# Kernel optimization log

Hardware: AMD Instinct MI355X
Metric: run time of the kernel (lower is better)

## Reference

```python
import jax, jax.numpy as jnp
import numpy as np

T = 8192
N_EMBD = 1024
HEAD_SIZE = 64
NEG_FILL = -1e9


def setup_inputs() -> dict:
    key = jax.random.key(0)
    kq, kk, kv, kwq, kwk, kwv = jax.random.split(key, 6)
    s = 1.0 / np.sqrt(N_EMBD)
    return {
        "encodings_for_q": jax.random.normal(kq, (T, N_EMBD), dtype=jnp.float32),
        "encodings_for_k": jax.random.normal(kk, (T, N_EMBD), dtype=jnp.float32),
        "encodings_for_v": jax.random.normal(kv, (T, N_EMBD), dtype=jnp.float32),
        # causal mask: True above the diagonal -> positions to mask out
        "mask": jnp.triu(jnp.ones((T, T), dtype=bool), k=1),
        # torch Linear weights have shape [out_features, in_features]
        "W_q": jax.random.normal(kwq, (HEAD_SIZE, N_EMBD), dtype=jnp.float32) * s,
        "W_k": jax.random.normal(kwk, (HEAD_SIZE, N_EMBD), dtype=jnp.float32) * s,
        "W_v": jax.random.normal(kwv, (HEAD_SIZE, N_EMBD), dtype=jnp.float32) * s,
    }


def reference(encodings_for_q, encodings_for_k, encodings_for_v, mask, W_q, W_k, W_v):
    # projections: x @ W.T  (torch nn.Linear, bias=False)
    q = jnp.einsum("te,he->th", encodings_for_q, W_q)  # [T, H]
    k = jnp.einsum("te,he->th", encodings_for_k, W_k)  # [T, H]
    v = jnp.einsum("te,he->th", encodings_for_v, W_v)  # [T, H]
    scale = 1.0 / jnp.sqrt(jnp.asarray(HEAD_SIZE, dtype=q.dtype))
    sims = jnp.einsum("th,sh->ts", q, k) * scale       # [T, T]
    sims = jnp.where(mask, jnp.asarray(NEG_FILL, dtype=sims.dtype), sims)
    attn = jax.nn.softmax(sims, axis=1)                # softmax over col_dim=1
    return jnp.einsum("ts,sh->th", attn, v)            # [T, H]
```

## Files before the change

### kernel.cpp

```cpp
#include <hip/hip_runtime.h>
#include <hip/hip_bf16.h>
#include <stdint.h>

#define T_DIM 8192
#define E_DIM 1024
#define H_DIM 64
#define NEGF  -3.0e38f

typedef __attribute__((ext_vector_type(8))) short bf16x8;
typedef __attribute__((ext_vector_type(4))) float f32x4;

static __device__ __forceinline__ uint32_t pk2(float x, float y) {
    __hip_bfloat162 h = __float22bfloat162_rn(make_float2(x, y));
    union { __hip_bfloat162 h2; uint32_t u; } c; c.h2 = h; return c.u;
}
static __device__ __forceinline__ bf16x8 pack8(float4 a, float4 b) {
    union { bf16x8 v; uint32_t u[4]; } c;
    c.u[0] = pk2(a.x, a.y); c.u[1] = pk2(a.z, a.w);
    c.u[2] = pk2(b.x, b.y); c.u[3] = pk2(b.z, b.w);
    return c.v;
}
static __device__ __forceinline__ uint16_t bf1(float x) {
    __hip_bfloat16 h = __float2bfloat16(x);
    union { __hip_bfloat16 h1; uint16_t s; } c; c.h1 = h; return c.s;
}

__global__ __launch_bounds__(256) void wconv_kernel(
    const float* __restrict__ Wq, const float* __restrict__ Wk, const float* __restrict__ Wv,
    uint16_t* __restrict__ Wqb, uint16_t* __restrict__ Wkb, uint16_t* __restrict__ Wvb)
{
    const int idx = blockIdx.x * 256 + threadIdx.x;
    const int which = idx / 16384;
    const int off = (idx & 16383) * 4;
    const float* W = (which == 0) ? Wq : (which == 1) ? Wk : Wv;
    uint16_t* Wb   = (which == 0) ? Wqb : (which == 1) ? Wkb : Wvb;
    float4 w = *(const float4*)(W + off);
    uint2 o = make_uint2(pk2(w.x, w.y), pk2(w.z, w.w));
    *(uint2*)(Wb + off) = o;
}

__global__ __launch_bounds__(256) void proj_kernel(
    const float* __restrict__ Xq, const float* __restrict__ Xk, const float* __restrict__ Xv,
    const uint16_t* __restrict__ Wqb, const uint16_t* __restrict__ Wkb, const uint16_t* __restrict__ Wvb,
    uint16_t* __restrict__ Qb, uint16_t* __restrict__ Kb, uint16_t* __restrict__ Vtb)
{
    __shared__ float TD[64][69];

    const int mat = blockIdx.y;
    const float* X    = (mat == 0) ? Xq  : (mat == 1) ? Xk  : Xv;
    const uint16_t* W = (mat == 0) ? Wqb : (mat == 1) ? Wkb : Wvb;

    const int tid  = threadIdx.x;
    const int wv   = tid >> 6;
    const int lane = tid & 63;
    const int lidx = lane & 15;
    const int quad = lane >> 4;
    const int t0   = blockIdx.x * 64 + wv * 16;

    const float* Xr = X + (size_t)(t0 + lidx) * E_DIM + quad * 8;

    f32x4 acc[4] = {{0,0,0,0},{0,0,0,0},{0,0,0,0},{0,0,0,0}};
    for (int k0 = 0; k0 < E_DIM; k0 += 32) {
        float4 x0 = *(const float4*)(Xr + k0);
        float4 x1 = *(const float4*)(Xr + k0 + 4);
        bf16x8 xa = pack8(x0, x1);
        #pragma unroll
        for (int nt = 0; nt < 4; ++nt) {
            const uint16_t* Wr = W + (size_t)(nt * 16 + lidx) * E_DIM + k0 + quad * 8;
            bf16x8 wb = *(const bf16x8*)Wr;
            acc[nt] = __builtin_amdgcn_mfma_f32_16x16x32_bf16(xa, wb, acc[nt], 0, 0, 0);
        }
    }

    if (mat < 2) {
        uint16_t* O = (mat == 0) ? Qb : Kb;
        #pragma unroll
        for (int nt = 0; nt < 4; ++nt)
            #pragma unroll
            for (int r = 0; r < 4; ++r)
                O[(size_t)(t0 + quad * 4 + r) * H_DIM + nt * 16 + lidx] = bf1(acc[nt][r]);
    } else {
        #pragma unroll
        for (int nt = 0; nt < 4; ++nt)
            #pragma unroll
            for (int r = 0; r < 4; ++r)
                TD[wv * 16 + quad * 4 + r][nt * 16 + lidx] = acc[nt][r];
        __syncthreads();
        const int h = tid >> 2, tq = tid & 3;
        uint32_t w8[8];
        #pragma unroll
        for (int i = 0; i < 8; ++i)
            w8[i] = pk2(TD[tq * 16 + 2 * i][h], TD[tq * 16 + 2 * i + 1][h]);
        uint16_t* dst = Vtb + (size_t)h * T_DIM + blockIdx.x * 64 + tq * 16;
        uint4 lo = make_uint4(w8[0], w8[1], w8[2], w8[3]);
        uint4 hi = make_uint4(w8[4], w8[5], w8[6], w8[7]);
        *(uint4*)dst       = lo;
        *(uint4*)(dst + 8) = hi;
    }
}

__global__ __launch_bounds__(512) void flash_kernel(
    const uint16_t* __restrict__ Qb, const uint16_t* __restrict__ Kb,
    const uint16_t* __restrict__ Vtb, float* __restrict__ Out)
{
    __shared__ __align__(16) float WS[8][16][68];
    __shared__ float Mw[8][16];
    __shared__ float Lw[8][16];

    const int tid  = threadIdx.x;
    const int wv   = tid >> 6;
    const int lane = tid & 63;
    const int lidx = lane & 15;
    const int quad = lane >> 4;

    const int qt = 511 - (int)blockIdx.x;
    const int q0 = qt * 16;

    bf16x8 aq0 = *(const bf16x8*)(Qb + (size_t)(q0 + lidx) * H_DIM + quad * 8);
    bf16x8 aq1 = *(const bf16x8*)(Qb + (size_t)(q0 + lidx) * H_DIM + 32 + quad * 8);

    const int ktiles  = qt / 4 + 1;
    const int base    = ktiles >> 3;
    const int rem     = ktiles & 7;
    const int myn     = base + (wv < rem ? 1 : 0);
    const int mystart = wv * base + (wv < rem ? wv : rem);

    float m[4] = {NEGF, NEGF, NEGF, NEGF};
    float l[4] = {0.f, 0.f, 0.f, 0.f};
    f32x4 o[4] = {{0,0,0,0},{0,0,0,0},{0,0,0,0},{0,0,0,0}};

    for (int it = 0; it < myn; ++it) {
        const int kt = mystart + it;
        const int s0 = kt * 64;

        f32x4 s[4];
        #pragma unroll
        for (int nt = 0; nt < 4; ++nt) {
            const uint16_t* kr = Kb + (size_t)(s0 + nt * 16 + lidx) * H_DIM + quad * 8;
            bf16x8 b0 = *(const bf16x8*)(kr);
            bf16x8 b1 = *(const bf16x8*)(kr + 32);
            f32x4 z = {0, 0, 0, 0};
            s[nt] = __builtin_amdgcn_mfma_f32_16x16x32_bf16(aq0, b0, z, 0, 0, 0);
            s[nt] = __builtin_amdgcn_mfma_f32_16x16x32_bf16(aq1, b1, s[nt], 0, 0, 0);
        }

        if (kt == ktiles - 1) {
            #pragma unroll
            for (int nt = 0; nt < 4; ++nt)
                #pragma unroll
                for (int r = 0; r < 4; ++r) {
                    const int col = s0 + nt * 16 + lidx;
                    const int row = q0 + quad * 4 + r;
                    s[nt][r] = (col <= row) ? s[nt][r] * 0.125f : NEGF;
                }
        } else {
            #pragma unroll
            for (int nt = 0; nt < 4; ++nt)
                #pragma unroll
                for (int r = 0; r < 4; ++r)
                    s[nt][r] *= 0.125f;
        }

        #pragma unroll
        for (int r = 0; r < 4; ++r) {
            float mt = fmaxf(fmaxf(s[0][r], s[1][r]), fmaxf(s[2][r], s[3][r]));
            mt = fmaxf(mt, __shfl_xor(mt, 1));
            mt = fmaxf(mt, __shfl_xor(mt, 2));
            mt = fmaxf(mt, __shfl_xor(mt, 4));
            mt = fmaxf(mt, __shfl_xor(mt, 8));
            const float mn = fmaxf(m[r], mt);
            const float al = __expf(m[r] - mn);
            m[r] = mn;
            float ps = 0.f;
            #pragma unroll
            for (int nt = 0; nt < 4; ++nt) {
                const float pv = __expf(s[nt][r] - mn);
                WS[wv][quad * 4 + r][nt * 16 + lidx] = pv;
                ps += pv;
            }
            ps += __shfl_xor(ps, 1);
            ps += __shfl_xor(ps, 2);
            ps += __shfl_xor(ps, 4);
            ps += __shfl_xor(ps, 8);
            l[r] = l[r] * al + ps;
            #pragma unroll
            for (int nt = 0; nt < 4; ++nt) o[nt][r] *= al;
        }

        const float* pr = &WS[wv][lidx][0];
        float4 p0 = *(const float4*)(pr + quad * 8);
        float4 p1 = *(const float4*)(pr + quad * 8 + 4);
        float4 p2 = *(const float4*)(pr + 32 + quad * 8);
        float4 p3 = *(const float4*)(pr + 32 + quad * 8 + 4);
        bf16x8 ap0 = pack8(p0, p1);
        bf16x8 ap1 = pack8(p2, p3);

        #pragma unroll
        for (int nt = 0; nt < 4; ++nt) {
            const uint16_t* vr = Vtb + (size_t)(nt * 16 + lidx) * T_DIM + s0 + quad * 8;
            bf16x8 v0 = *(const bf16x8*)(vr);
            bf16x8 v1 = *(const bf16x8*)(vr + 32);
            o[nt] = __builtin_amdgcn_mfma_f32_16x16x32_bf16(ap0, v0, o[nt], 0, 0, 0);
            o[nt] = __builtin_amdgcn_mfma_f32_16x16x32_bf16(ap1, v1, o[nt], 0, 0, 0);
        }
    }

    if (lidx == 0) {
        #pragma unroll
        for (int r = 0; r < 4; ++r) { Mw[wv][quad * 4 + r] = m[r]; Lw[wv][quad * 4 + r] = l[r]; }
    }
    #pragma unroll
    for (int nt = 0; nt < 4; ++nt)
        #pragma unroll
        for (int r = 0; r < 4; ++r)
            WS[wv][quad * 4 + r][nt * 16 + lidx] = o[nt][r];
    __syncthreads();

    const int row = tid >> 5, cg = tid & 31;
    float M = NEGF;
    #pragma unroll
    for (int w2 = 0; w2 < 8; ++w2) M = fmaxf(M, Mw[w2][row]);
    float L = 0.f;
    float ox = 0.f, oy = 0.f;
    #pragma unroll
    for (int w2 = 0; w2 < 8; ++w2) {
        const float sc = __expf(Mw[w2][row] - M);
        L += Lw[w2][row] * sc;
        float2 t = *(const float2*)&WS[w2][row][cg * 2];
        ox += t.x * sc; oy += t.y * sc;
    }
    const float inv = 1.f / L;
    *(float2*)(Out + (size_t)(q0 + row) * H_DIM + cg * 2) = make_float2(ox * inv, oy * inv);
}

extern "C" void kernel_launch(void* const* d_in, const int* in_sizes, int n_in,
                              void* d_out, int out_size, void* d_ws, size_t ws_size,
                              hipStream_t stream) {
    (void)in_sizes; (void)n_in; (void)out_size; (void)ws_size;
    const float* Xq = (const float*)d_in[0];
    const float* Xk = (const float*)d_in[1];
    const float* Xv = (const float*)d_in[2];
    const float* Wq = (const float*)d_in[4];
    const float* Wk = (const float*)d_in[5];
    const float* Wv = (const float*)d_in[6];

    uint16_t* Qb  = (uint16_t*)d_ws;
    uint16_t* Kb  = Qb + (size_t)T_DIM * H_DIM;
    uint16_t* Vtb = Kb + (size_t)T_DIM * H_DIM;
    uint16_t* Wqb = Vtb + (size_t)T_DIM * H_DIM;
    uint16_t* Wkb = Wqb + (size_t)H_DIM * E_DIM;
    uint16_t* Wvb = Wkb + (size_t)H_DIM * E_DIM;

    wconv_kernel<<<192, 256, 0, stream>>>(Wq, Wk, Wv, Wqb, Wkb, Wvb);

    dim3 pgrid(T_DIM / 64, 3);
    proj_kernel<<<pgrid, 256, 0, stream>>>(Xq, Xk, Xv, Wqb, Wkb, Wvb, Qb, Kb, Vtb);

    flash_kernel<<<T_DIM / 16, 512, 0, stream>>>(Qb, Kb, Vtb, (float*)d_out);
}
```

Before: 467.0 us.

## Split-K projection, fold softmax scale into Wq, prefetch K/V, defer row sums

```diff
diff --git a/kernel.cpp b/kernel.cpp
--- a/kernel.cpp
+++ b/kernel.cpp
@@ -6,6 +6,7 @@
 #define E_DIM 1024
 #define H_DIM 64
 #define NEGF  -3.0e38f
+#define QSCALE 0.18033688011112042f
 
 typedef __attribute__((ext_vector_type(8))) short bf16x8;
 typedef __attribute__((ext_vector_type(4))) float f32x4;
@@ -34,16 +35,18 @@
     const int off = (idx & 16383) * 4;
     const float* W = (which == 0) ? Wq : (which == 1) ? Wk : Wv;
     uint16_t* Wb   = (which == 0) ? Wqb : (which == 1) ? Wkb : Wvb;
+    const float s  = (which == 0) ? QSCALE : 1.0f;
     float4 w = *(const float4*)(W + off);
-    uint2 o = make_uint2(pk2(w.x, w.y), pk2(w.z, w.w));
+    uint2 o = make_uint2(pk2(w.x * s, w.y * s), pk2(w.z * s, w.w * s));
     *(uint2*)(Wb + off) = o;
 }
 
-__global__ __launch_bounds__(256) void proj_kernel(
+__global__ __launch_bounds__(512) void proj_kernel(
     const float* __restrict__ Xq, const float* __restrict__ Xk, const float* __restrict__ Xv,
     const uint16_t* __restrict__ Wqb, const uint16_t* __restrict__ Wkb, const uint16_t* __restrict__ Wvb,
     uint16_t* __restrict__ Qb, uint16_t* __restrict__ Kb, uint16_t* __restrict__ Vtb)
 {
+    __shared__ float PS[4][16][68];
     __shared__ float TD[64][69];
 
     const int mat = blockIdx.y;
@@ -52,50 +55,73 @@
 
     const int tid  = threadIdx.x;
     const int wv   = tid >> 6;
+    const int rs   = wv & 3;
+    const int kh   = wv >> 2;
     const int lane = tid & 63;
     const int lidx = lane & 15;
     const int quad = lane >> 4;
-    const int t0   = blockIdx.x * 64 + wv * 16;
-
-    const float* Xr = X + (size_t)(t0 + lidx) * E_DIM + quad * 8;
+    const int t0   = blockIdx.x * 64 + rs * 16;
+
+    const float*    Xr  = X + (size_t)(t0 + lidx) * E_DIM + kh * 512 + quad * 8;
+    const uint16_t* Wr0 = W + (size_t)lidx * E_DIM + kh * 512 + quad * 8;
 
     f32x4 acc[4] = {{0,0,0,0},{0,0,0,0},{0,0,0,0},{0,0,0,0}};
-    for (int k0 = 0; k0 < E_DIM; k0 += 32) {
+    #pragma unroll 4
+    for (int k0 = 0; k0 < 512; k0 += 32) {
         float4 x0 = *(const float4*)(Xr + k0);
         float4 x1 = *(const float4*)(Xr + k0 + 4);
         bf16x8 xa = pack8(x0, x1);
         #pragma unroll
         for (int nt = 0; nt < 4; ++nt) {
-            const uint16_t* Wr = W + (size_t)(nt * 16 + lidx) * E_DIM + k0 + quad * 8;
-            bf16x8 wb = *(const bf16x8*)Wr;
+            bf16x8 wb = *(const bf16x8*)(Wr0 + (size_t)nt * 16 * E_DIM + k0);
             acc[nt] = __builtin_amdgcn_mfma_f32_16x16x32_bf16(xa, wb, acc[nt], 0, 0, 0);
         }
     }
 
-    if (mat < 2) {
-        uint16_t* O = (mat == 0) ? Qb : Kb;
+    if (kh) {
         #pragma unroll
         for (int nt = 0; nt < 4; ++nt)
             #pragma unroll
             for (int r = 0; r < 4; ++r)
-                O[(size_t)(t0 + quad * 4 + r) * H_DIM + nt * 16 + lidx] = bf1(acc[nt][r]);
-    } else {
+                PS[rs][quad * 4 + r][nt * 16 + lidx] = acc[nt][r];
+    }
+    __syncthreads();
+    if (!kh) {
         #pragma unroll
         for (int nt = 0; nt < 4; ++nt)
             #pragma unroll
             for (int r = 0; r < 4; ++r)
-                TD[wv * 16 + quad * 4 + r][nt * 16 + lidx] = acc[nt][r];
+                acc[nt][r] += PS[rs][quad * 4 + r][nt * 16 + lidx];
+
+        if (mat < 2) {
+            uint16_t* O = (mat == 0) ? Qb : Kb;
+            #pragma unroll
+            for (int nt = 0; nt < 4; ++nt)
+                #pragma unroll
+                for (int r = 0; r < 4; ++r)
+                    O[(size_t)(t0 + quad * 4 + r) * H_DIM + nt * 16 + lidx] = bf1(acc[nt][r]);
+        } else {
+            #pragma unroll
+            for (int nt = 0; nt < 4; ++nt)
+                #pragma unroll
+                for (int r = 0; r < 4; ++r)
+                    TD[rs * 16 + quad * 4 + r][nt * 16 + lidx] = acc[nt][r];
+        }
+    }
+    if (mat == 2) {
         __syncthreads();
-        const int h = tid >> 2, tq = tid & 3;
-        uint32_t w8[8];
-        #pragma unroll
-        for (int i = 0; i < 8; ++i)
-            w8[i] = pk2(TD[tq * 16 + 2 * i][h], TD[tq * 16 + 2 * i + 1][h]);
-        uint16_t* dst = Vtb + (size_t)h * T_DIM + blockIdx.x * 64 + tq * 16;
-        uint4 lo = make_uint4(w8[0], w8[1], w8[2], w8[3]);
-        uint4 hi = make_uint4(w8[4], w8[5], w8[6], w8[7]);
-        *(uint4*)dst       = lo;
-        *(uint4*)(dst + 8) = hi;
+        if (tid < 256) {
+            const int h = tid >> 2, tq = tid & 3;
+            uint32_t w8[8];
+            #pragma unroll
+            for (int i = 0; i < 8; ++i)
+                w8[i] = pk2(TD[tq * 16 + 2 * i][h], TD[tq * 16 + 2 * i + 1][h]);
+            uint16_t* dst = Vtb + (size_t)h * T_DIM + blockIdx.x * 64 + tq * 16;
+            uint4 lo = make_uint4(w8[0], w8[1], w8[2], w8[3]);
+            uint4 hi = make_uint4(w8[4], w8[5], w8[6], w8[7]);
+            *(uint4*)dst       = lo;
+            *(uint4*)(dst + 8) = hi;
+        }
     }
 }
 
@@ -129,19 +155,50 @@
     float l[4] = {0.f, 0.f, 0.f, 0.f};
     f32x4 o[4] = {{0,0,0,0},{0,0,0,0},{0,0,0,0},{0,0,0,0}};
 
+    const uint16_t* Kl = Kb  + (size_t)lidx * H_DIM + quad * 8;
+    const uint16_t* Vl = Vtb + (size_t)lidx * T_DIM + quad * 8;
+
+    bf16x8 kb[8];
+    if (myn > 0) {
+        const int s0 = mystart * 64;
+        #pragma unroll
+        for (int nt = 0; nt < 4; ++nt) {
+            const uint16_t* kr = Kl + (size_t)(s0 + nt * 16) * H_DIM;
+            kb[2 * nt]     = *(const bf16x8*)kr;
+            kb[2 * nt + 1] = *(const bf16x8*)(kr + 32);
+        }
+    }
+
     for (int it = 0; it < myn; ++it) {
         const int kt = mystart + it;
         const int s0 = kt * 64;
 
+        bf16x8 vb[8];
+        #pragma unroll
+        for (int nt = 0; nt < 4; ++nt) {
+            const uint16_t* vr = Vl + (size_t)(nt * 16) * T_DIM + s0;
+            vb[2 * nt]     = *(const bf16x8*)vr;
+            vb[2 * nt + 1] = *(const bf16x8*)(vr + 32);
+        }
+
         f32x4 s[4];
-        #pragma unroll
-        for (int nt = 0; nt < 4; ++nt) {
-            const uint16_t* kr = Kb + (size_t)(s0 + nt * 16 + lidx) * H_DIM + quad * 8;
-            bf16x8 b0 = *(const bf16x8*)(kr);
-            bf16x8 b1 = *(const bf16x8*)(kr + 32);
+        __builtin_amdgcn_s_setprio(1);
+        #pragma unroll
+        for (int nt = 0; nt < 4; ++nt) {
             f32x4 z = {0, 0, 0, 0};
-            s[nt] = __builtin_amdgcn_mfma_f32_16x16x32_bf16(aq0, b0, z, 0, 0, 0);
-            s[nt] = __builtin_amdgcn_mfma_f32_16x16x32_bf16(aq1, b1, s[nt], 0, 0, 0);
+            s[nt] = __builtin_amdgcn_mfma_f32_16x16x32_bf16(aq0, kb[2 * nt],     z,     0, 0, 0);
+            s[nt] = __builtin_amdgcn_mfma_f32_16x16x32_bf16(aq1, kb[2 * nt + 1], s[nt], 0, 0, 0);
+        }
+        __builtin_amdgcn_s_setprio(0);
+
+        {
+            const int s0n = ((it + 1 < myn) ? (kt + 1) : kt) * 64;
+            #pragma unroll
+            for (int nt = 0; nt < 4; ++nt) {
+                const uint16_t* kr = Kl + (size_t)(s0n + nt * 16) * H_DIM;
+                kb[2 * nt]     = *(const bf16x8*)kr;
+                kb[2 * nt + 1] = *(const bf16x8*)(kr + 32);
+            }
         }
 
         if (kt == ktiles - 1) {
@@ -151,14 +208,8 @@
                 for (int r = 0; r < 4; ++r) {
                     const int col = s0 + nt * 16 + lidx;
                     const int row = q0 + quad * 4 + r;
-                    s[nt][r] = (col <= row) ? s[nt][r] * 0.125f : NEGF;
+                    s[nt][r] = (col <= row) ? s[nt][r] : NEGF;
                 }
-        } else {
-            #pragma unroll
-            for (int nt = 0; nt < 4; ++nt)
-                #pragma unroll
-                for (int r = 0; r < 4; ++r)
-                    s[nt][r] *= 0.125f;
         }
 
         #pragma unroll
@@ -169,19 +220,15 @@
             mt = fmaxf(mt, __shfl_xor(mt, 4));
             mt = fmaxf(mt, __shfl_xor(mt, 8));
             const float mn = fmaxf(m[r], mt);
-            const float al = __expf(m[r] - mn);
+            const float al = exp2f(m[r] - mn);
             m[r] = mn;
             float ps = 0.f;
             #pragma unroll
             for (int nt = 0; nt < 4; ++nt) {
-                const float pv = __expf(s[nt][r] - mn);
+                const float pv = exp2f(s[nt][r] - mn);
                 WS[wv][quad * 4 + r][nt * 16 + lidx] = pv;
                 ps += pv;
             }
-            ps += __shfl_xor(ps, 1);
-            ps += __shfl_xor(ps, 2);
-            ps += __shfl_xor(ps, 4);
-            ps += __shfl_xor(ps, 8);
             l[r] = l[r] * al + ps;
             #pragma unroll
             for (int nt = 0; nt < 4; ++nt) o[nt][r] *= al;
@@ -195,14 +242,23 @@
         bf16x8 ap0 = pack8(p0, p1);
         bf16x8 ap1 = pack8(p2, p3);
 
-        #pragma unroll
-        for (int nt = 0; nt < 4; ++nt) {
-            const uint16_t* vr = Vtb + (size_t)(nt * 16 + lidx) * T_DIM + s0 + quad * 8;
-            bf16x8 v0 = *(const bf16x8*)(vr);
-            bf16x8 v1 = *(const bf16x8*)(vr + 32);
-            o[nt] = __builtin_amdgcn_mfma_f32_16x16x32_bf16(ap0, v0, o[nt], 0, 0, 0);
-            o[nt] = __builtin_amdgcn_mfma_f32_16x16x32_bf16(ap1, v1, o[nt], 0, 0, 0);
-        }
+        __builtin_amdgcn_s_setprio(1);
+        #pragma unroll
+        for (int nt = 0; nt < 4; ++nt) {
+            o[nt] = __builtin_amdgcn_mfma_f32_16x16x32_bf16(ap0, vb[2 * nt],     o[nt], 0, 0, 0);
+            o[nt] = __builtin_amdgcn_mfma_f32_16x16x32_bf16(ap1, vb[2 * nt + 1], o[nt], 0, 0, 0);
+        }
+        __builtin_amdgcn_s_setprio(0);
+    }
+
+    #pragma unroll
+    for (int r = 0; r < 4; ++r) {
+        float ps = l[r];
+        ps += __shfl_xor(ps, 1);
+        ps += __shfl_xor(ps, 2);
+        ps += __shfl_xor(ps, 4);
+        ps += __shfl_xor(ps, 8);
+        l[r] = ps;
     }
 
     if (lidx == 0) {
@@ -224,7 +280,7 @@
     float ox = 0.f, oy = 0.f;
     #pragma unroll
     for (int w2 = 0; w2 < 8; ++w2) {
-        const float sc = __expf(Mw[w2][row] - M);
+        const float sc = exp2f(Mw[w2][row] - M);
         L += Lw[w2][row] * sc;
         float2 t = *(const float2*)&WS[w2][row][cg * 2];
         ox += t.x * sc; oy += t.y * sc;
@@ -254,7 +310,7 @@
     wconv_kernel<<<192, 256, 0, stream>>>(Wq, Wk, Wv, Wqb, Wkb, Wvb);
 
     dim3 pgrid(T_DIM / 64, 3);
-    proj_kernel<<<pgrid, 256, 0, stream>>>(Xq, Xk, Xv, Wqb, Wkb, Wvb, Qb, Kb, Vtb);
+    proj_kernel<<<pgrid, 512, 0, stream>>>(Xq, Xk, Xv, Wqb, Wkb, Wvb, Qb, Kb, Vtb);
 
     flash_kernel<<<T_DIM / 16, 512, 0, stream>>>(Qb, Kb, Vtb, (float*)d_out);
 }
```

New measurement: 451.2 us. 3.4% less time.
